# Optimization experiments

Measured on AMD Instinct MI355X. Metric: run time of the kernel, lower is better.

Reference implementation:

```python
import jax, jax.numpy as jnp
import numpy as np

B, T, C = 2, 2048, 1024
NH, NKV, HD = 16, 4, 64
VEC = 32  # ve_gate_channels


def _rope(x, cos, sin):
    d = x.shape[-1] // 2
    x1, x2 = x[..., :d], x[..., d:]
    return jnp.concatenate([x1 * cos + x2 * sin, -x1 * sin + x2 * cos], axis=-1)


def _rmsnorm(x):
    eps = jnp.finfo(x.dtype).eps
    return x * jax.lax.rsqrt(jnp.mean(x * x, axis=-1, keepdims=True) + eps)


def setup_inputs() -> dict:
    key = jax.random.key(0)
    ks = jax.random.split(key, 9)
    s = 0.02
    return {
        "x": jax.random.normal(ks[0], (B, T, C), jnp.float32),
        "ve": jax.random.normal(ks[1], (B, T, NKV * HD), jnp.float32),
        "cos": jax.random.normal(ks[2], (1, T, 1, HD // 2), jnp.float32),
        "sin": jax.random.normal(ks[3], (1, T, 1, HD // 2), jnp.float32),
        "Wq": jax.random.normal(ks[4], (C, NH * HD), jnp.float32) * s,
        "Wk": jax.random.normal(ks[5], (C, NKV * HD), jnp.float32) * s,
        "Wv": jax.random.normal(ks[6], (C, NKV * HD), jnp.float32) * s,
        "Wproj": jax.random.normal(ks[7], (C, C), jnp.float32) * s,
        "Wgate": jax.random.normal(ks[8], (VEC, NKV), jnp.float32) * s,
        "window_size": 1024,
    }


def reference(x, ve, cos, sin, Wq, Wk, Wv, Wproj, Wgate, window_size):
    Bx, Tx, Cx = x.shape
    q = (x @ Wq).reshape(Bx, Tx, NH, HD)
    k = (x @ Wk).reshape(Bx, Tx, NKV, HD)
    v = (x @ Wv).reshape(Bx, Tx, NKV, HD)

    # value-embedding gate (has_ve True for this layer)
    gate = 2.0 * jax.nn.sigmoid(x[..., :VEC] @ Wgate)  # [B,T,NKV]
    v = v + gate[..., None] * ve.reshape(Bx, Tx, NKV, HD)

    q, k = _rope(q, cos, sin), _rope(k, cos, sin)
    q, k = _rmsnorm(q), _rmsnorm(k)

    q = q.transpose(0, 2, 1, 3)  # [B,NH,T,HD]
    k = k.transpose(0, 2, 1, 3)  # [B,NKV,T,HD]
    v = v.transpose(0, 2, 1, 3)

    # GQA: each KV head serves NH//NKV consecutive q heads
    g = NH // NKV
    k = jnp.repeat(k, g, axis=1)
    v = jnp.repeat(v, g, axis=1)

    row = jnp.arange(Tx)[:, None]
    col = jnp.arange(Tx)[None, :]
    mask = (col <= row) & (col >= row - window_size)  # causal sliding window

    scores = jnp.einsum("bhqd,bhkd->bhqk", q, k) / np.sqrt(HD).astype(np.float32)
    scores = jnp.where(mask[None, None], scores, jnp.finfo(scores.dtype).min)
    attn = jax.nn.softmax(scores, axis=-1)
    y = jnp.einsum("bhqk,bhkd->bhqd", attn, v)

    y = y.transpose(0, 2, 1, 3).reshape(Bx, Tx, Cx)
    return y @ Wproj
```

## Files before the change

### kernel.cpp

```cpp
#include <hip/hip_runtime.h>

typedef __bf16 bf16x8 __attribute__((ext_vector_type(8)));
typedef float f32x4 __attribute__((ext_vector_type(4)));

__device__ inline float tof(float v) { return v; }
__device__ inline float tof(__bf16 v) { return (float)v; }

__device__ inline bf16x8 load8(const __bf16* p) { return *(const bf16x8*)p; }
__device__ inline bf16x8 load8(const float* p) {
    const float4 a = *(const float4*)p;
    const float4 b = *(const float4*)(p + 4);
    bf16x8 r;
    r[0] = (__bf16)a.x; r[1] = (__bf16)a.y; r[2] = (__bf16)a.z; r[3] = (__bf16)a.w;
    r[4] = (__bf16)b.x; r[5] = (__bf16)b.y; r[6] = (__bf16)b.z; r[7] = (__bf16)b.w;
    return r;
}

__device__ __forceinline__ void cp16(__bf16* lds, const __bf16* g) {
    __builtin_amdgcn_global_load_lds((__attribute__((address_space(1))) void*)g,
                                     (__attribute__((address_space(3))) void*)lds,
                                     16, 0, 0);
}

__global__ void sniff_kernel(const unsigned short* __restrict__ xs, int* flag) {
    if (threadIdx.x != 0) return;
    int bad = 0;
    for (int i = 0; i < 512; ++i) {
        unsigned int f = ((unsigned int)xs[i]) << 16;
        float v = __uint_as_float(f);
        float a = fabsf(v);
        if (!(a <= 1e4f) || (a != 0.f && a < 1e-6f)) bad++;
    }
    *flag = (bad > 32) ? 1 : 0;
}

template <typename T>
__global__ __launch_bounds__(256) void prep_kernel(
    const T* __restrict__ x, const T* __restrict__ ve,
    const T* __restrict__ cosp, const T* __restrict__ sinp,
    const T* __restrict__ Wq, const T* __restrict__ Wk,
    const T* __restrict__ Wv, const T* __restrict__ Wp, const T* __restrict__ Wg,
    __bf16* __restrict__ xb, __bf16* __restrict__ veb,
    float* __restrict__ cosf_, float* __restrict__ sinf_,
    __bf16* __restrict__ WqT, __bf16* __restrict__ WkT,
    __bf16* __restrict__ WvT, __bf16* __restrict__ WpT,
    float* __restrict__ gate, const int* __restrict__ flag)
{
    if (*flag != (int)(sizeof(T) == 4)) return;
    __shared__ __bf16 tile[64 * 72];
    const int b = blockIdx.x, tid = threadIdx.x;

    if (b < 2624) {
        int g = b * 256 + tid;
        if (g < 524288) {
            *(bf16x8*)(xb + (size_t)g * 8) = load8(x + (size_t)g * 8);
        } else if (g < 655360) {
            int gg = g - 524288;
            *(bf16x8*)(veb + (size_t)gg * 8) = load8(ve + (size_t)gg * 8);
        } else if (g < 663552) {
            int gg = g - 655360;
            const T* s = cosp + (size_t)gg * 8; float* d = cosf_ + (size_t)gg * 8;
#pragma unroll
            for (int j = 0; j < 8; ++j) d[j] = tof(s[j]);
        } else {
            int gg = g - 663552;
            const T* s = sinp + (size_t)gg * 8; float* d = sinf_ + (size_t)gg * 8;
#pragma unroll
            for (int j = 0; j < 8; ++j) d[j] = tof(s[j]);
        }
    } else if (b < 3264) {
        int idx = b - 2624;
        const T* src; __bf16* dst; int C;
        if (idx < 256)      { src = Wq; dst = WqT; C = 1024; }
        else if (idx < 320) { src = Wk; dst = WkT; C = 256;  idx -= 256; }
        else if (idx < 384) { src = Wv; dst = WvT; C = 256;  idx -= 320; }
        else                { src = Wp; dst = WpT; C = 1024; idx -= 384; }
        const int ctiles = C >> 6;
        const int r0 = (idx / ctiles) * 64, c0 = (idx % ctiles) * 64;
#pragma unroll
        for (int i = 0; i < 2; ++i) {
            int c = tid + i * 256, ir = c >> 3, ic = (c & 7) * 8;
            *(bf16x8*)(&tile[ir * 72 + ic]) = load8(src + (size_t)(r0 + ir) * C + c0 + ic);
        }
        __syncthreads();
#pragma unroll
        for (int i = 0; i < 2; ++i) {
            int c = tid + i * 256, orr = c >> 3, okc = (c & 7) * 8;
            bf16x8 v;
#pragma unroll
            for (int j = 0; j < 8; ++j) v[j] = tile[(okc + j) * 72 + orr];
            *(bf16x8*)(dst + (size_t)(c0 + orr) * 1024 + r0 + okc) = v;
        }
    } else {
        int r = (b - 3264) * 256 + tid;
        float z[4] = {0.f, 0.f, 0.f, 0.f};
        for (int j = 0; j < 32; ++j) {
            float xv = tof(x[(size_t)r * 1024 + j]);
#pragma unroll
            for (int h = 0; h < 4; ++h) z[h] += xv * tof(Wg[j * 4 + h]);
        }
#pragma unroll
        for (int h = 0; h < 4; ++h) gate[r * 4 + h] = 2.f / (1.f + __expf(-z[h]));
    }
}

__global__ __launch_bounds__(256) void qkv_kernel(
    const __bf16* __restrict__ xb,
    const __bf16* __restrict__ WqT, const __bf16* __restrict__ WkT,
    const __bf16* __restrict__ WvT, const __bf16* __restrict__ veb,
    const float* __restrict__ cosf_, const float* __restrict__ sinf_,
    const float* __restrict__ gate,
    __bf16* __restrict__ qo, __bf16* __restrict__ ko, __bf16* __restrict__ vo)
{
    const int row0 = blockIdx.x * 128;
    const int cb = blockIdx.y;
    const __bf16* BT; int col0, mode;
    if (cb < 8)       { BT = WqT; col0 = cb * 128;        mode = 0; }
    else if (cb < 10) { BT = WkT; col0 = (cb - 8) * 128;  mode = 1; }
    else              { BT = WvT; col0 = (cb - 10) * 128; mode = 2; }

    __shared__ __align__(16) __bf16 As[128 * 32];
    __shared__ __align__(16) __bf16 Bs[128 * 32];

    const int tid  = threadIdx.x;
    const int w    = tid >> 6;
    const int lane = tid & 63;
    const int quad = lane >> 4;
    const int l15  = lane & 15;
    const int wr   = (w >> 1) * 64, wc = (w & 1) * 64;

    f32x4 acc[4][4];
#pragma unroll
    for (int mi = 0; mi < 4; ++mi)
#pragma unroll
        for (int nj = 0; nj < 4; ++nj) acc[mi][nj] = (f32x4){0.f, 0.f, 0.f, 0.f};

    for (int kk = 0; kk < 1024; kk += 32) {
#pragma unroll
        for (int i = 0; i < 2; ++i) {
            int c = i * 256 + (w << 6) + lane;
            int rr = c >> 2, kc = (c & 3) << 3;
            cp16(&As[c << 3], &xb[(size_t)(row0 + rr) * 1024 + kk + kc]);
            cp16(&Bs[c << 3], &BT[(size_t)(col0 + rr) * 1024 + kk + kc]);
        }
        __syncthreads();
        bf16x8 a[4], bfr[4];
#pragma unroll
        for (int mi = 0; mi < 4; ++mi) a[mi]  = *(const bf16x8*)(&As[(wr + mi * 16 + l15) * 32 + quad * 8]);
#pragma unroll
        for (int nj = 0; nj < 4; ++nj) bfr[nj] = *(const bf16x8*)(&Bs[(wc + nj * 16 + l15) * 32 + quad * 8]);
#pragma unroll
        for (int mi = 0; mi < 4; ++mi)
#pragma unroll
            for (int nj = 0; nj < 4; ++nj)
                acc[mi][nj] = __builtin_amdgcn_mfma_f32_16x16x32_bf16(a[mi], bfr[nj], acc[mi][nj], 0, 0, 0);
        __syncthreads();
    }

    const int h = (col0 + wc) >> 6;
    if (mode < 2) {
        __bf16* dst = (mode == 0) ? qo : ko;
        const int nh = (mode == 0) ? 16 : 4;
#pragma unroll
        for (int mi = 0; mi < 4; ++mi) {
#pragma unroll
            for (int r = 0; r < 4; ++r) {
                int row = row0 + wr + mi * 16 + quad * 4 + r;
                int b = row >> 11, t = row & 2047;
                float c0 = cosf_[t * 32 + l15];
                float c1 = cosf_[t * 32 + 16 + l15];
                float s0 = sinf_[t * 32 + l15];
                float s1 = sinf_[t * 32 + 16 + l15];
                float v0 =  c0 * acc[mi][0][r] + s0 * acc[mi][2][r];
                float v1 =  c1 * acc[mi][1][r] + s1 * acc[mi][3][r];
                float v2 = -s0 * acc[mi][0][r] + c0 * acc[mi][2][r];
                float v3 = -s1 * acc[mi][1][r] + c1 * acc[mi][3][r];
                float ss = v0 * v0 + v1 * v1 + v2 * v2 + v3 * v3;
                ss += __shfl_xor(ss, 1); ss += __shfl_xor(ss, 2);
                ss += __shfl_xor(ss, 4); ss += __shfl_xor(ss, 8);
                float sc = rsqrtf(ss * (1.f / 64.f) + 1.1920929e-7f);
                size_t base = (((size_t)b * nh + h) * 2048 + t) * 64;
                dst[base + 0 * 16 + l15] = (__bf16)(v0 * sc);
                dst[base + 1 * 16 + l15] = (__bf16)(v1 * sc);
                dst[base + 2 * 16 + l15] = (__bf16)(v2 * sc);
                dst[base + 3 * 16 + l15] = (__bf16)(v3 * sc);
            }
        }
    } else {
#pragma unroll
        for (int mi = 0; mi < 4; ++mi) {
#pragma unroll
            for (int r = 0; r < 4; ++r) {
                int row = row0 + wr + mi * 16 + quad * 4 + r;
                int b = row >> 11, t = row & 2047;
                float g = gate[row * 4 + h];
                size_t obase = (((size_t)b * 4 + h) * 2048 + t) * 64;
#pragma unroll
                for (int nj = 0; nj < 4; ++nj) {
                    float val = acc[mi][nj][r] + g * tof(veb[(size_t)row * 256 + h * 64 + nj * 16 + l15]);
                    vo[obase + nj * 16 + l15] = (__bf16)val;
                }
            }
        }
    }
}

__global__ __launch_bounds__(256) void attn_kernel(
    const __bf16* __restrict__ qg, const __bf16* __restrict__ kg,
    const __bf16* __restrict__ vg, __bf16* __restrict__ yo,
    const int* __restrict__ winp)
{
    const int qt = blockIdx.x, hh = blockIdx.y, b = blockIdx.z;
    const int q0 = qt * 64;
    const int kvh = hh >> 2;
    const int W = winp[0];

    const int tid  = threadIdx.x;
    const int w    = tid >> 6;
    const int lane = tid & 63;
    const int quad = lane >> 4;
    const int l15  = lane & 15;

    __shared__ __align__(16) __bf16 Ks[2][64 * 72];
    __shared__ __align__(16) __bf16 Vt[2][64 * 72];
    __shared__ __align__(16) __bf16 Ps[4][16 * 72];

    const size_t qbase = (((size_t)b * 16 + hh) * 2048 + q0 + w * 16 + l15) * 64;
    bf16x8 qf0 = *(const bf16x8*)(&qg[qbase + quad * 8]);
    bf16x8 qf1 = *(const bf16x8*)(&qg[qbase + 32 + quad * 8]);

    f32x4 oacc[4];
#pragma unroll
    for (int n = 0; n < 4; ++n) oacc[n] = (f32x4){0.f, 0.f, 0.f, 0.f};
    float lsum[4] = {0.f, 0.f, 0.f, 0.f};

    int lo = q0 - W;
    const int kt_lo = lo > 0 ? (lo >> 6) : 0;
    const size_t kbase = ((size_t)b * 4 + kvh) * 2048 * 64;

    {
        const int k0 = kt_lo * 64;
#pragma unroll
        for (int i = 0; i < 2; ++i) {
            int c = i * 256 + tid;
            int rk = c >> 3, dk = (c & 7) * 8;
            bf16x8 kv = *(const bf16x8*)(&kg[kbase + (size_t)(k0 + rk) * 64 + dk]);
            *(bf16x8*)(&Ks[0][rk * 72 + dk]) = kv;
            int rv = c & 63, dv = ((c >> 6) & 7) * 8;
            bf16x8 vv = *(const bf16x8*)(&vg[kbase + (size_t)(k0 + rv) * 64 + dv]);
#pragma unroll
            for (int j = 0; j < 8; ++j) Vt[0][(dv + j) * 72 + rv] = vv[j];
        }
    }
    __syncthreads();

    int cur = 0;
    for (int kt = kt_lo; kt <= qt; ++kt) {
        const int k0 = kt * 64;
        const bool need_mask = (kt == qt) || (q0 + 63 - k0 > W);
        const bool pf = (kt < qt);
        bf16x8 pk[2], pv[2];
        if (pf) {
            const int k0n = k0 + 64;
#pragma unroll
            for (int i = 0; i < 2; ++i) {
                int c = i * 256 + tid;
                int rk = c >> 3, dk = (c & 7) * 8;
                pk[i] = *(const bf16x8*)(&kg[kbase + (size_t)(k0n + rk) * 64 + dk]);
                int rv = c & 63, dv = ((c >> 6) & 7) * 8;
                pv[i] = *(const bf16x8*)(&vg[kbase + (size_t)(k0n + rv) * 64 + dv]);
            }
        }

        f32x4 sacc[4];
#pragma unroll
        for (int n = 0; n < 4; ++n) sacc[n] = (f32x4){0.f, 0.f, 0.f, 0.f};
        const __bf16* Kc = &Ks[cur][0];
#pragma unroll
        for (int n = 0; n < 4; ++n) {
            bf16x8 b0 = *(const bf16x8*)(&Kc[(n * 16 + l15) * 72 + quad * 8]);
            sacc[n] = __builtin_amdgcn_mfma_f32_16x16x32_bf16(qf0, b0, sacc[n], 0, 0, 0);
            bf16x8 b1 = *(const bf16x8*)(&Kc[(n * 16 + l15) * 72 + 32 + quad * 8]);
            sacc[n] = __builtin_amdgcn_mfma_f32_16x16x32_bf16(qf1, b1, sacc[n], 0, 0, 0);
        }

#pragma unroll
        for (int r = 0; r < 4; ++r) {
            const int row_g = q0 + w * 16 + quad * 4 + r;
#pragma unroll
            for (int n = 0; n < 4; ++n) {
                float p = exp2f(fmaf(sacc[n][r], 0.18033688f, -11.5415603f));
                if (need_mask) {
                    int col_g = k0 + n * 16 + l15;
                    bool ok = (col_g <= row_g) && (row_g - col_g <= W);
                    p = ok ? p : 0.f;
                }
                lsum[r] += p;
                Ps[w][(quad * 4 + r) * 72 + n * 16 + l15] = (__bf16)p;
            }
        }
        asm volatile("s_waitcnt lgkmcnt(0)" ::: "memory");

        const __bf16* Vc = &Vt[cur][0];
#pragma unroll
        for (int ks = 0; ks < 2; ++ks) {
            bf16x8 pfr = *(const bf16x8*)(&Ps[w][l15 * 72 + ks * 32 + quad * 8]);
#pragma unroll
            for (int n = 0; n < 4; ++n) {
                bf16x8 bv = *(const bf16x8*)(&Vc[(n * 16 + l15) * 72 + ks * 32 + quad * 8]);
                oacc[n] = __builtin_amdgcn_mfma_f32_16x16x32_bf16(pfr, bv, oacc[n], 0, 0, 0);
            }
        }

        if (pf) {
            const int nxt = cur ^ 1;
#pragma unroll
            for (int i = 0; i < 2; ++i) {
                int c = i * 256 + tid;
                int rk = c >> 3, dk = (c & 7) * 8;
                *(bf16x8*)(&Ks[nxt][rk * 72 + dk]) = pk[i];
                int rv = c & 63, dv = ((c >> 6) & 7) * 8;
#pragma unroll
                for (int j = 0; j < 8; ++j) Vt[nxt][(dv + j) * 72 + rv] = pv[i][j];
            }
            cur = nxt;
        }
        __syncthreads();
    }

#pragma unroll
    for (int r = 0; r < 4; ++r) {
        float l = lsum[r];
        l += __shfl_xor(l, 1); l += __shfl_xor(l, 2);
        l += __shfl_xor(l, 4); l += __shfl_xor(l, 8);
        float inv = 1.f / l;
        int t = q0 + w * 16 + quad * 4 + r;
        size_t base = ((size_t)(b * 2048 + t)) * 1024 + hh * 64;
#pragma unroll
        for (int n = 0; n < 4; ++n)
            yo[base + n * 16 + l15] = (__bf16)(oacc[n][r] * inv);
    }
}

template <typename T>
__global__ __launch_bounds__(256) void proj_kernel(
    const __bf16* __restrict__ y, const __bf16* __restrict__ WpT,
    T* __restrict__ out, const int* __restrict__ flag)
{
    if (*flag != (int)(sizeof(T) == 4)) return;
    const int row0 = blockIdx.x * 128;
    const int col0 = blockIdx.y * 128;
    __shared__ __align__(16) __bf16 As[128 * 32];
    __shared__ __align__(16) __bf16 Bs[128 * 32];

    const int tid  = threadIdx.x;
    const int w    = tid >> 6;
    const int lane = tid & 63;
    const int quad = lane >> 4;
    const int l15  = lane & 15;
    const int wr   = (w >> 1) * 64, wc = (w & 1) * 64;

    f32x4 acc[4][4];
#pragma unroll
    for (int mi = 0; mi < 4; ++mi)
#pragma unroll
        for (int nj = 0; nj < 4; ++nj) acc[mi][nj] = (f32x4){0.f, 0.f, 0.f, 0.f};

    for (int kk = 0; kk < 1024; kk += 32) {
#pragma unroll
        for (int i = 0; i < 2; ++i) {
            int c = i * 256 + (w << 6) + lane;
            int rr = c >> 2, kc = (c & 3) << 3;
            cp16(&As[c << 3], &y[(size_t)(row0 + rr) * 1024 + kk + kc]);
            cp16(&Bs[c << 3], &WpT[(size_t)(col0 + rr) * 1024 + kk + kc]);
        }
        __syncthreads();
        bf16x8 a[4], bfr[4];
#pragma unroll
        for (int mi = 0; mi < 4; ++mi) a[mi]  = *(const bf16x8*)(&As[(wr + mi * 16 + l15) * 32 + quad * 8]);
#pragma unroll
        for (int nj = 0; nj < 4; ++nj) bfr[nj] = *(const bf16x8*)(&Bs[(wc + nj * 16 + l15) * 32 + quad * 8]);
#pragma unroll
        for (int mi = 0; mi < 4; ++mi)
#pragma unroll
            for (int nj = 0; nj < 4; ++nj)
                acc[mi][nj] = __builtin_amdgcn_mfma_f32_16x16x32_bf16(a[mi], bfr[nj], acc[mi][nj], 0, 0, 0);
        __syncthreads();
    }

#pragma unroll
    for (int mi = 0; mi < 4; ++mi)
#pragma unroll
        for (int r = 0; r < 4; ++r) {
            int row = row0 + wr + mi * 16 + quad * 4 + r;
#pragma unroll
            for (int nj = 0; nj < 4; ++nj)
                out[(size_t)row * 1024 + col0 + wc + nj * 16 + l15] = (T)acc[mi][nj][r];
        }
}

extern "C" void kernel_launch(void* const* d_in, const int* in_sizes, int n_in,
                              void* d_out, int out_size, void* d_ws, size_t ws_size,
                              hipStream_t stream) {
    const int* win = (const int*)d_in[9];

    char* p = (char*)d_ws;
    int*    flag = (int*)p;                    p += 256;
    __bf16* q_ws = (__bf16*)p;                 p += (size_t)4194304 * 2;
    __bf16* k_ws = (__bf16*)p;                 p += (size_t)1048576 * 2;
    __bf16* v_ws = (__bf16*)p;                 p += (size_t)1048576 * 2;
    __bf16* y_ws = (__bf16*)p;                 p += (size_t)4194304 * 2;
    __bf16* xb   = (__bf16*)p;                 p += (size_t)4194304 * 2;
    __bf16* veb  = (__bf16*)p;                 p += (size_t)1048576 * 2;
    __bf16* WqT  = (__bf16*)p;                 p += (size_t)1048576 * 2;
    __bf16* WkT  = (__bf16*)p;                 p += (size_t)262144 * 2;
    __bf16* WvT  = (__bf16*)p;                 p += (size_t)262144 * 2;
    __bf16* WpT  = (__bf16*)p;                 p += (size_t)1048576 * 2;
    float*  cosf_ = (float*)p;                 p += (size_t)65536 * 4;
    float*  sinf_ = (float*)p;                 p += (size_t)65536 * 4;
    float*  gate  = (float*)p;                 p += (size_t)16384 * 4;

    sniff_kernel<<<1, 64, 0, stream>>>((const unsigned short*)d_in[0], flag);

    prep_kernel<float><<<3280, 256, 0, stream>>>(
        (const float*)d_in[0], (const float*)d_in[1], (const float*)d_in[2],
        (const float*)d_in[3], (const float*)d_in[4], (const float*)d_in[5],
        (const float*)d_in[6], (const float*)d_in[7], (const float*)d_in[8],
        xb, veb, cosf_, sinf_, WqT, WkT, WvT, WpT, gate, flag);
    prep_kernel<__bf16><<<3280, 256, 0, stream>>>(
        (const __bf16*)d_in[0], (const __bf16*)d_in[1], (const __bf16*)d_in[2],
        (const __bf16*)d_in[3], (const __bf16*)d_in[4], (const __bf16*)d_in[5],
        (const __bf16*)d_in[6], (const __bf16*)d_in[7], (const __bf16*)d_in[8],
        xb, veb, cosf_, sinf_, WqT, WkT, WvT, WpT, gate, flag);

    qkv_kernel<<<dim3(32, 12), 256, 0, stream>>>(xb, WqT, WkT, WvT, veb,
                                                 cosf_, sinf_, gate, q_ws, k_ws, v_ws);

    attn_kernel<<<dim3(32, 16, 2), 256, 0, stream>>>(q_ws, k_ws, v_ws, y_ws, win);

    proj_kernel<float><<<dim3(32, 8), 256, 0, stream>>>(y_ws, WpT, (float*)d_out, flag);
    proj_kernel<__bf16><<<dim3(32, 8), 256, 0, stream>>>(y_ws, WpT, (__bf16*)d_out, flag);
}
```

Measured before the change: 232.1 us.

## Merge dtype kernel pairs, shrink GEMM tiles, enlarge attention query tile

The float and bf16 variants of the prep and proj kernels are merged into single launches that branch on the runtime dtype flag, which drops two empty kernel launches. The QKV and output-projection GEMMs go from 128x128 to 128x64 tiles, doubling the grid to fill more compute units at the cost of less operand reuse per block. The attention kernel now handles 128 queries per block (32 per wave), so each K/V tile loaded into shared memory serves twice as many queries. That halves the attention grid and raises register and LDS use per block.

Result: faster. 213.2 us (-8.1%).

```diff
diff --git a/kernel.cpp b/kernel.cpp
--- a/kernel.cpp
+++ b/kernel.cpp
@@ -35,7 +35,7 @@
 }
 
 template <typename T>
-__global__ __launch_bounds__(256) void prep_kernel(
+__device__ __forceinline__ void prep_body(
     const T* __restrict__ x, const T* __restrict__ ve,
     const T* __restrict__ cosp, const T* __restrict__ sinp,
     const T* __restrict__ Wq, const T* __restrict__ Wk,
@@ -44,10 +44,8 @@
     float* __restrict__ cosf_, float* __restrict__ sinf_,
     __bf16* __restrict__ WqT, __bf16* __restrict__ WkT,
     __bf16* __restrict__ WvT, __bf16* __restrict__ WpT,
-    float* __restrict__ gate, const int* __restrict__ flag)
+    float* __restrict__ gate, __bf16* tile)
 {
-    if (*flag != (int)(sizeof(T) == 4)) return;
-    __shared__ __bf16 tile[64 * 72];
     const int b = blockIdx.x, tid = threadIdx.x;
 
     if (b < 2624) {
@@ -104,6 +102,27 @@
     }
 }
 
+__global__ __launch_bounds__(256) void prep_kernel(
+    const void* x, const void* ve, const void* cosp, const void* sinp,
+    const void* Wq, const void* Wk, const void* Wv, const void* Wp, const void* Wg,
+    __bf16* xb, __bf16* veb, float* cosf_, float* sinf_,
+    __bf16* WqT, __bf16* WkT, __bf16* WvT, __bf16* WpT,
+    float* gate, const int* __restrict__ flag)
+{
+    __shared__ __bf16 tile[64 * 72];
+    if (*flag) {
+        prep_body<float>((const float*)x, (const float*)ve, (const float*)cosp,
+                         (const float*)sinp, (const float*)Wq, (const float*)Wk,
+                         (const float*)Wv, (const float*)Wp, (const float*)Wg,
+                         xb, veb, cosf_, sinf_, WqT, WkT, WvT, WpT, gate, tile);
+    } else {
+        prep_body<__bf16>((const __bf16*)x, (const __bf16*)ve, (const __bf16*)cosp,
+                          (const __bf16*)sinp, (const __bf16*)Wq, (const __bf16*)Wk,
+                          (const __bf16*)Wv, (const __bf16*)Wp, (const __bf16*)Wg,
+                          xb, veb, cosf_, sinf_, WqT, WkT, WvT, WpT, gate, tile);
+    }
+}
+
 __global__ __launch_bounds__(256) void qkv_kernel(
     const __bf16* __restrict__ xb,
     const __bf16* __restrict__ WqT, const __bf16* __restrict__ WkT,
@@ -114,24 +133,24 @@
 {
     const int row0 = blockIdx.x * 128;
     const int cb = blockIdx.y;
-    const __bf16* BT; int col0, mode;
-    if (cb < 8)       { BT = WqT; col0 = cb * 128;        mode = 0; }
-    else if (cb < 10) { BT = WkT; col0 = (cb - 8) * 128;  mode = 1; }
-    else              { BT = WvT; col0 = (cb - 10) * 128; mode = 2; }
+    const __bf16* BT; int col0, h, mode;
+    if (cb < 16)      { BT = WqT; col0 = cb * 64;        h = cb;      mode = 0; }
+    else if (cb < 20) { BT = WkT; col0 = (cb - 16) * 64; h = cb - 16; mode = 1; }
+    else              { BT = WvT; col0 = (cb - 20) * 64; h = cb - 20; mode = 2; }
 
     __shared__ __align__(16) __bf16 As[128 * 32];
-    __shared__ __align__(16) __bf16 Bs[128 * 32];
+    __shared__ __align__(16) __bf16 Bs[64 * 32];
 
     const int tid  = threadIdx.x;
     const int w    = tid >> 6;
     const int lane = tid & 63;
     const int quad = lane >> 4;
     const int l15  = lane & 15;
-    const int wr   = (w >> 1) * 64, wc = (w & 1) * 64;
-
-    f32x4 acc[4][4];
-#pragma unroll
-    for (int mi = 0; mi < 4; ++mi)
+    const int wr   = w * 32;
+
+    f32x4 acc[2][4];
+#pragma unroll
+    for (int mi = 0; mi < 2; ++mi)
 #pragma unroll
         for (int nj = 0; nj < 4; ++nj) acc[mi][nj] = (f32x4){0.f, 0.f, 0.f, 0.f};
 
@@ -141,28 +160,31 @@
             int c = i * 256 + (w << 6) + lane;
             int rr = c >> 2, kc = (c & 3) << 3;
             cp16(&As[c << 3], &xb[(size_t)(row0 + rr) * 1024 + kk + kc]);
+        }
+        {
+            int c = (w << 6) + lane;
+            int rr = c >> 2, kc = (c & 3) << 3;
             cp16(&Bs[c << 3], &BT[(size_t)(col0 + rr) * 1024 + kk + kc]);
         }
         __syncthreads();
-        bf16x8 a[4], bfr[4];
-#pragma unroll
-        for (int mi = 0; mi < 4; ++mi) a[mi]  = *(const bf16x8*)(&As[(wr + mi * 16 + l15) * 32 + quad * 8]);
-#pragma unroll
-        for (int nj = 0; nj < 4; ++nj) bfr[nj] = *(const bf16x8*)(&Bs[(wc + nj * 16 + l15) * 32 + quad * 8]);
-#pragma unroll
-        for (int mi = 0; mi < 4; ++mi)
+        bf16x8 a[2], bfr[4];
+#pragma unroll
+        for (int mi = 0; mi < 2; ++mi) a[mi]  = *(const bf16x8*)(&As[(wr + mi * 16 + l15) * 32 + quad * 8]);
+#pragma unroll
+        for (int nj = 0; nj < 4; ++nj) bfr[nj] = *(const bf16x8*)(&Bs[(nj * 16 + l15) * 32 + quad * 8]);
+#pragma unroll
+        for (int mi = 0; mi < 2; ++mi)
 #pragma unroll
             for (int nj = 0; nj < 4; ++nj)
                 acc[mi][nj] = __builtin_amdgcn_mfma_f32_16x16x32_bf16(a[mi], bfr[nj], acc[mi][nj], 0, 0, 0);
         __syncthreads();
     }
 
-    const int h = (col0 + wc) >> 6;
     if (mode < 2) {
         __bf16* dst = (mode == 0) ? qo : ko;
         const int nh = (mode == 0) ? 16 : 4;
 #pragma unroll
-        for (int mi = 0; mi < 4; ++mi) {
+        for (int mi = 0; mi < 2; ++mi) {
 #pragma unroll
             for (int r = 0; r < 4; ++r) {
                 int row = row0 + wr + mi * 16 + quad * 4 + r;
@@ -188,7 +210,7 @@
         }
     } else {
 #pragma unroll
-        for (int mi = 0; mi < 4; ++mi) {
+        for (int mi = 0; mi < 2; ++mi) {
 #pragma unroll
             for (int r = 0; r < 4; ++r) {
                 int row = row0 + wr + mi * 16 + quad * 4 + r;
@@ -210,8 +232,8 @@
     const __bf16* __restrict__ vg, __bf16* __restrict__ yo,
     const int* __restrict__ winp)
 {
-    const int qt = blockIdx.x, hh = blockIdx.y, b = blockIdx.z;
-    const int q0 = qt * 64;
+    const int q0 = blockIdx.x * 128;
+    const int hh = blockIdx.y, b = blockIdx.z;
     const int kvh = hh >> 2;
     const int W = winp[0];
 
@@ -223,19 +245,29 @@
 
     __shared__ __align__(16) __bf16 Ks[2][64 * 72];
     __shared__ __align__(16) __bf16 Vt[2][64 * 72];
-    __shared__ __align__(16) __bf16 Ps[4][16 * 72];
-
-    const size_t qbase = (((size_t)b * 16 + hh) * 2048 + q0 + w * 16 + l15) * 64;
-    bf16x8 qf0 = *(const bf16x8*)(&qg[qbase + quad * 8]);
-    bf16x8 qf1 = *(const bf16x8*)(&qg[qbase + 32 + quad * 8]);
-
-    f32x4 oacc[4];
-#pragma unroll
-    for (int n = 0; n < 4; ++n) oacc[n] = (f32x4){0.f, 0.f, 0.f, 0.f};
-    float lsum[4] = {0.f, 0.f, 0.f, 0.f};
-
-    int lo = q0 - W;
+    __shared__ __align__(16) __bf16 Ps[4][32 * 72];
+
+    bf16x8 qf[2][2];
+#pragma unroll
+    for (int i = 0; i < 2; ++i) {
+        size_t qb = (((size_t)b * 16 + hh) * 2048 + q0 + w * 32 + i * 16 + l15) * 64;
+        qf[i][0] = *(const bf16x8*)(&qg[qb + quad * 8]);
+        qf[i][1] = *(const bf16x8*)(&qg[qb + 32 + quad * 8]);
+    }
+
+    f32x4 oacc[2][4];
+    float lsum[2][4];
+#pragma unroll
+    for (int i = 0; i < 2; ++i)
+#pragma unroll
+        for (int n = 0; n < 4; ++n) {
+            oacc[i][n] = (f32x4){0.f, 0.f, 0.f, 0.f};
+            lsum[i][n] = 0.f;
+        }
+
+    const int lo = q0 - W;
     const int kt_lo = lo > 0 ? (lo >> 6) : 0;
+    const int kt_hi = (q0 + 127) >> 6;
     const size_t kbase = ((size_t)b * 4 + kvh) * 2048 * 64;
 
     {
@@ -255,10 +287,10 @@
     __syncthreads();
 
     int cur = 0;
-    for (int kt = kt_lo; kt <= qt; ++kt) {
+    for (int kt = kt_lo; kt <= kt_hi; ++kt) {
         const int k0 = kt * 64;
-        const bool need_mask = (kt == qt) || (q0 + 63 - k0 > W);
-        const bool pf = (kt < qt);
+        const bool need_mask = (k0 + 63 > q0) || (q0 + 127 - k0 > W);
+        const bool pf = (kt < kt_hi);
         bf16x8 pk[2], pv[2];
         if (pf) {
             const int k0n = k0 + 64;
@@ -272,31 +304,39 @@
             }
         }
 
-        f32x4 sacc[4];
-#pragma unroll
-        for (int n = 0; n < 4; ++n) sacc[n] = (f32x4){0.f, 0.f, 0.f, 0.f};
+        f32x4 sacc[2][4];
+#pragma unroll
+        for (int i = 0; i < 2; ++i)
+#pragma unroll
+            for (int n = 0; n < 4; ++n) sacc[i][n] = (f32x4){0.f, 0.f, 0.f, 0.f};
         const __bf16* Kc = &Ks[cur][0];
 #pragma unroll
         for (int n = 0; n < 4; ++n) {
             bf16x8 b0 = *(const bf16x8*)(&Kc[(n * 16 + l15) * 72 + quad * 8]);
-            sacc[n] = __builtin_amdgcn_mfma_f32_16x16x32_bf16(qf0, b0, sacc[n], 0, 0, 0);
             bf16x8 b1 = *(const bf16x8*)(&Kc[(n * 16 + l15) * 72 + 32 + quad * 8]);
-            sacc[n] = __builtin_amdgcn_mfma_f32_16x16x32_bf16(qf1, b1, sacc[n], 0, 0, 0);
-        }
-
-#pragma unroll
-        for (int r = 0; r < 4; ++r) {
-            const int row_g = q0 + w * 16 + quad * 4 + r;
-#pragma unroll
-            for (int n = 0; n < 4; ++n) {
-                float p = exp2f(fmaf(sacc[n][r], 0.18033688f, -11.5415603f));
-                if (need_mask) {
-                    int col_g = k0 + n * 16 + l15;
-                    bool ok = (col_g <= row_g) && (row_g - col_g <= W);
-                    p = ok ? p : 0.f;
+#pragma unroll
+            for (int i = 0; i < 2; ++i) {
+                sacc[i][n] = __builtin_amdgcn_mfma_f32_16x16x32_bf16(qf[i][0], b0, sacc[i][n], 0, 0, 0);
+                sacc[i][n] = __builtin_amdgcn_mfma_f32_16x16x32_bf16(qf[i][1], b1, sacc[i][n], 0, 0, 0);
+            }
+        }
+
+#pragma unroll
+        for (int i = 0; i < 2; ++i) {
+#pragma unroll
+            for (int r = 0; r < 4; ++r) {
+                const int row_g = q0 + w * 32 + i * 16 + quad * 4 + r;
+#pragma unroll
+                for (int n = 0; n < 4; ++n) {
+                    float p = exp2f(fmaf(sacc[i][n][r], 0.18033688f, -11.5415603f));
+                    if (need_mask) {
+                        int col_g = k0 + n * 16 + l15;
+                        bool ok = (col_g <= row_g) && (row_g - col_g <= W);
+                        p = ok ? p : 0.f;
+                    }
+                    lsum[i][r] += p;
+                    Ps[w][(i * 16 + quad * 4 + r) * 72 + n * 16 + l15] = (__bf16)p;
                 }
-                lsum[r] += p;
-                Ps[w][(quad * 4 + r) * 72 + n * 16 + l15] = (__bf16)p;
             }
         }
         asm volatile("s_waitcnt lgkmcnt(0)" ::: "memory");
@@ -304,11 +344,13 @@
         const __bf16* Vc = &Vt[cur][0];
 #pragma unroll
         for (int ks = 0; ks < 2; ++ks) {
-            bf16x8 pfr = *(const bf16x8*)(&Ps[w][l15 * 72 + ks * 32 + quad * 8]);
+            bf16x8 pfr0 = *(const bf16x8*)(&Ps[w][l15 * 72 + ks * 32 + quad * 8]);
+            bf16x8 pfr1 = *(const bf16x8*)(&Ps[w][(16 + l15) * 72 + ks * 32 + quad * 8]);
 #pragma unroll
             for (int n = 0; n < 4; ++n) {
                 bf16x8 bv = *(const bf16x8*)(&Vc[(n * 16 + l15) * 72 + ks * 32 + quad * 8]);
-                oacc[n] = __builtin_amdgcn_mfma_f32_16x16x32_bf16(pfr, bv, oacc[n], 0, 0, 0);
+                oacc[0][n] = __builtin_amdgcn_mfma_f32_16x16x32_bf16(pfr0, bv, oacc[0][n], 0, 0, 0);
+                oacc[1][n] = __builtin_amdgcn_mfma_f32_16x16x32_bf16(pfr1, bv, oacc[1][n], 0, 0, 0);
             }
         }
 
@@ -329,40 +371,42 @@
     }
 
 #pragma unroll
-    for (int r = 0; r < 4; ++r) {
-        float l = lsum[r];
-        l += __shfl_xor(l, 1); l += __shfl_xor(l, 2);
-        l += __shfl_xor(l, 4); l += __shfl_xor(l, 8);
-        float inv = 1.f / l;
-        int t = q0 + w * 16 + quad * 4 + r;
-        size_t base = ((size_t)(b * 2048 + t)) * 1024 + hh * 64;
-#pragma unroll
-        for (int n = 0; n < 4; ++n)
-            yo[base + n * 16 + l15] = (__bf16)(oacc[n][r] * inv);
-    }
-}
-
-template <typename T>
+    for (int i = 0; i < 2; ++i) {
+#pragma unroll
+        for (int r = 0; r < 4; ++r) {
+            float l = lsum[i][r];
+            l += __shfl_xor(l, 1); l += __shfl_xor(l, 2);
+            l += __shfl_xor(l, 4); l += __shfl_xor(l, 8);
+            float inv = 1.f / l;
+            int t = q0 + w * 32 + i * 16 + quad * 4 + r;
+            size_t base = ((size_t)(b * 2048 + t)) * 1024 + hh * 64;
+#pragma unroll
+            for (int n = 0; n < 4; ++n)
+                yo[base + n * 16 + l15] = (__bf16)(oacc[i][n][r] * inv);
+        }
+    }
+}
+
 __global__ __launch_bounds__(256) void proj_kernel(
     const __bf16* __restrict__ y, const __bf16* __restrict__ WpT,
-    T* __restrict__ out, const int* __restrict__ flag)
+    void* __restrict__ outp, const int* __restrict__ flag)
 {
-    if (*flag != (int)(sizeof(T) == 4)) return;
+    const int isf32 = *flag;
     const int row0 = blockIdx.x * 128;
-    const int col0 = blockIdx.y * 128;
+    const int col0 = blockIdx.y * 64;
     __shared__ __align__(16) __bf16 As[128 * 32];
-    __shared__ __align__(16) __bf16 Bs[128 * 32];
+    __shared__ __align__(16) __bf16 Bs[64 * 32];
 
     const int tid  = threadIdx.x;
     const int w    = tid >> 6;
     const int lane = tid & 63;
     const int quad = lane >> 4;
     const int l15  = lane & 15;
-    const int wr   = (w >> 1) * 64, wc = (w & 1) * 64;
-
-    f32x4 acc[4][4];
-#pragma unroll
-    for (int mi = 0; mi < 4; ++mi)
+    const int wr   = w * 32;
+
+    f32x4 acc[2][4];
+#pragma unroll
+    for (int mi = 0; mi < 2; ++mi)
 #pragma unroll
         for (int nj = 0; nj < 4; ++nj) acc[mi][nj] = (f32x4){0.f, 0.f, 0.f, 0.f};
 
@@ -372,16 +416,20 @@
             int c = i * 256 + (w << 6) + lane;
             int rr = c >> 2, kc = (c & 3) << 3;
             cp16(&As[c << 3], &y[(size_t)(row0 + rr) * 1024 + kk + kc]);
+        }
+        {
+            int c = (w << 6) + lane;
+            int rr = c >> 2, kc = (c & 3) << 3;
             cp16(&Bs[c << 3], &WpT[(size_t)(col0 + rr) * 1024 + kk + kc]);
         }
         __syncthreads();
-        bf16x8 a[4], bfr[4];
-#pragma unroll
-        for (int mi = 0; mi < 4; ++mi) a[mi]  = *(const bf16x8*)(&As[(wr + mi * 16 + l15) * 32 + quad * 8]);
-#pragma unroll
-        for (int nj = 0; nj < 4; ++nj) bfr[nj] = *(const bf16x8*)(&Bs[(wc + nj * 16 + l15) * 32 + quad * 8]);
-#pragma unroll
-        for (int mi = 0; mi < 4; ++mi)
+        bf16x8 a[2], bfr[4];
+#pragma unroll
+        for (int mi = 0; mi < 2; ++mi) a[mi]  = *(const bf16x8*)(&As[(wr + mi * 16 + l15) * 32 + quad * 8]);
+#pragma unroll
+        for (int nj = 0; nj < 4; ++nj) bfr[nj] = *(const bf16x8*)(&Bs[(nj * 16 + l15) * 32 + quad * 8]);
+#pragma unroll
+        for (int mi = 0; mi < 2; ++mi)
 #pragma unroll
             for (int nj = 0; nj < 4; ++nj)
                 acc[mi][nj] = __builtin_amdgcn_mfma_f32_16x16x32_bf16(a[mi], bfr[nj], acc[mi][nj], 0, 0, 0);
@@ -389,13 +437,21 @@
     }
 
 #pragma unroll
-    for (int mi = 0; mi < 4; ++mi)
+    for (int mi = 0; mi < 2; ++mi)
 #pragma unroll
         for (int r = 0; r < 4; ++r) {
             int row = row0 + wr + mi * 16 + quad * 4 + r;
-#pragma unroll
-            for (int nj = 0; nj < 4; ++nj)
-                out[(size_t)row * 1024 + col0 + wc + nj * 16 + l15] = (T)acc[mi][nj][r];
+            if (isf32) {
+                float* out = (float*)outp;
+#pragma unroll
+                for (int nj = 0; nj < 4; ++nj)
+                    out[(size_t)row * 1024 + col0 + nj * 16 + l15] = acc[mi][nj][r];
+            } else {
+                __bf16* out = (__bf16*)outp;
+#pragma unroll
+                for (int nj = 0; nj < 4; ++nj)
+                    out[(size_t)row * 1024 + col0 + nj * 16 + l15] = (__bf16)acc[mi][nj][r];
+            }
         }
 }
 
@@ -422,22 +478,14 @@
 
     sniff_kernel<<<1, 64, 0, stream>>>((const unsigned short*)d_in[0], flag);
 
-    prep_kernel<float><<<3280, 256, 0, stream>>>(
-        (const float*)d_in[0], (const float*)d_in[1], (const float*)d_in[2],
-        (const float*)d_in[3], (const float*)d_in[4], (const float*)d_in[5],
-        (const float*)d_in[6], (const float*)d_in[7], (const float*)d_in[8],
-        xb, veb, cosf_, sinf_, WqT, WkT, WvT, WpT, gate, flag);
-    prep_kernel<__bf16><<<3280, 256, 0, stream>>>(
-        (const __bf16*)d_in[0], (const __bf16*)d_in[1], (const __bf16*)d_in[2],
-        (const __bf16*)d_in[3], (const __bf16*)d_in[4], (const __bf16*)d_in[5],
-        (const __bf16*)d_in[6], (const __bf16*)d_in[7], (const __bf16*)d_in[8],
-        xb, veb, cosf_, sinf_, WqT, WkT, WvT, WpT, gate, flag);
-
-    qkv_kernel<<<dim3(32, 12), 256, 0, stream>>>(xb, WqT, WkT, WvT, veb,
+    prep_kernel<<<3280, 256, 0, stream>>>(
+        d_in[0], d_in[1], d_in[2], d_in[3], d_in[4], d_in[5], d_in[6], d_in[7],
+        d_in[8], xb, veb, cosf_, sinf_, WqT, WkT, WvT, WpT, gate, flag);
+
+    qkv_kernel<<<dim3(32, 24), 256, 0, stream>>>(xb, WqT, WkT, WvT, veb,
                                                  cosf_, sinf_, gate, q_ws, k_ws, v_ws);
 
-    attn_kernel<<<dim3(32, 16, 2), 256, 0, stream>>>(q_ws, k_ws, v_ws, y_ws, win);
-
-    proj_kernel<float><<<dim3(32, 8), 256, 0, stream>>>(y_ws, WpT, (float*)d_out, flag);
-    proj_kernel<__bf16><<<dim3(32, 8), 256, 0, stream>>>(y_ws, WpT, (__bf16*)d_out, flag);
-}
+    attn_kernel<<<dim3(16, 16, 2), 256, 0, stream>>>(q_ws, k_ws, v_ws, y_ws, win);
+
+    proj_kernel<<<dim3(32, 16), 256, 0, stream>>>(y_ws, WpT, d_out, flag);
+}
```
